# Optimization experiments

Measured on AMD Instinct MI355X. Metric: run time of the kernel, lower is better.

Reference implementation:

```python
import jax, jax.numpy as jnp
import numpy as np
import math

B, S, DM, H, F = 2, 2048, 1024, 16, 192  # F = head_dim init arg; per-head dim = F // 3
DH = F // 3
MAX_BIAS = 8.0


def _get_slopes(n):
    # faithful to ALiBiBias._get_slopes
    def pow2(n):
        start = 2.0 ** (-(2.0 ** (-(math.log2(n) - 3))))
        return [start * start ** i for i in range(n)]
    if math.log2(n).is_integer():
        return pow2(n)
    cp2 = 2 ** math.floor(math.log2(n))
    return pow2(cp2) + _get_slopes(2 * cp2)[0::2][: n - cp2]


def _rope_sin_cos(seq_len, dim):
    inv_freq = 1.0 / (10000.0 ** (jnp.arange(0, dim, 2, dtype=jnp.float32) / dim))
    freqs = jnp.outer(jnp.arange(seq_len, dtype=jnp.float32), inv_freq)  # [S, dim/2]
    # repeat(sin[:,None,:],2,axis=1).reshape(S,-1) == concat([sin,sin],-1)
    sin = jnp.concatenate([jnp.sin(freqs), jnp.sin(freqs)], axis=-1)  # [S, dim]
    cos = jnp.concatenate([jnp.cos(freqs), jnp.cos(freqs)], axis=-1)
    return sin, cos


def _rotate_half(x):
    x1, x2 = jnp.split(x, 2, axis=-1)
    return jnp.concatenate([-x2, x1], axis=-1)


def setup_inputs() -> dict:
    key = jax.random.key(0)
    kx, kq, ko = jax.random.split(key, 3)
    x = jax.random.normal(kx, (B, S, DM), dtype=jnp.float32)
    w_qkv = jax.random.normal(kq, (DM, H, F), dtype=jnp.float32) * (1.0 / math.sqrt(DM))
    b_qkv = jnp.zeros((H, F), dtype=jnp.float32)
    w_out = jax.random.normal(ko, (H, DH, DM), dtype=jnp.float32) * (1.0 / math.sqrt(H * DH))
    b_out = jnp.zeros((DM,), dtype=jnp.float32)
    return {"x": x, "w_qkv": w_qkv, "b_qkv": b_qkv, "w_out": w_out, "b_out": b_out}


def reference(x, w_qkv, b_qkv, w_out, b_out):
    b, s, dm = x.shape
    h, f = w_qkv.shape[1], w_qkv.shape[2]
    dh = f // 3
    # fused QKV projection: [B,S,H,F], then 3-way split on the feature axis
    qkv = jnp.einsum('bsd,dhf->bshf', x, w_qkv) + b_qkv
    q, k, v = jnp.split(qkv, 3, axis=-1)  # each [B,S,H,DH]
    # RoPE (rotate_half convention), broadcast over heads
    sin, cos = _rope_sin_cos(s, dh)
    sin, cos = sin[:, None, :], cos[:, None, :]  # [S,1,DH]
    q = q * cos + _rotate_half(q) * sin
    k = k * cos + _rotate_half(k) * sin
    # [B,H,S,DH]
    q = q.transpose(0, 2, 1, 3)
    k = k.transpose(0, 2, 1, 3)
    v = v.transpose(0, 2, 1, 3)
    # scores scaled by sqrt(head_dim init arg), as in the original non-flash path
    scores = jnp.einsum('bhqd,bhkd->bhqk', q, k) / jnp.sqrt(jnp.float32(f))
    # ALiBi bias
    slopes = jnp.asarray(_get_slopes(h), dtype=jnp.float32)  # [H]
    pos = jnp.arange(s, dtype=jnp.float32)
    rel = pos[None, :] - pos[:, None]  # j - i
    rel = jnp.where(rel > 0, 0.0, rel)
    alibi = rel[None, :, :] * slopes[:, None, None] * MAX_BIAS  # [H,S,S]
    scores = scores + alibi[None]  # [B,H,S,S]
    # causal mask
    causal = jnp.tril(jnp.ones((s, s), dtype=jnp.float32))
    scores = jnp.where(causal == 0, -1e9, scores)
    weights = jax.nn.softmax(scores, axis=-1)
    attn = jnp.einsum('bhqk,bhkd->bhqd', weights, v).transpose(0, 2, 1, 3)  # [B,S,H,DH]
    return jnp.einsum('bshd,hdm->bsm', attn, w_out) + b_out
```

## Files before the change

### kernel.cpp

```cpp
#include <hip/hip_runtime.h>
#include <math.h>

static constexpr int B_  = 2;
static constexpr int S_  = 2048;
static constexpr int H_  = 16;
static constexpr int DH_ = 64;
static constexpr float SCALE_ = 0.07216878364870322f;

typedef __attribute__((ext_vector_type(8))) short short8;
typedef __attribute__((ext_vector_type(4))) float floatx4;

__device__ __forceinline__ float bf2f(unsigned short u) {
    union { unsigned int i; float f; } c; c.i = ((unsigned int)u) << 16; return c.f;
}
__device__ __forceinline__ unsigned short f2bf(float f) {
    union { float f; unsigned int i; } c; c.f = f;
    unsigned int x = c.i;
    unsigned int r = (x + 0x7fffu + ((x >> 16) & 1u)) >> 16;
    if ((x & 0x7f800000u) == 0x7f800000u) r = x >> 16;
    return (unsigned short)r;
}
__device__ __forceinline__ unsigned short f2bf_pos(float f) {
    union { float f; unsigned int i; } c; c.f = f;
    return (unsigned short)((c.i + 0x7fffu + ((c.i >> 16) & 1u)) >> 16);
}
__device__ __forceinline__ void load_lds16(const unsigned short* g, unsigned short* l) {
    __builtin_amdgcn_global_load_lds(
        (const __attribute__((address_space(1))) unsigned int*)g,
        (__attribute__((address_space(3))) unsigned int*)l, 16, 0, 0);
}

__global__ __launch_bounds__(256) void cvt_x(
    const float* __restrict__ in, unsigned short* __restrict__ out)
{
    const int i = blockIdx.x * 256 + threadIdx.x;
    const float4 v = reinterpret_cast<const float4*>(in)[i];
    ushort4 r;
    r.x = f2bf(v.x); r.y = f2bf(v.y); r.z = f2bf(v.z); r.w = f2bf(v.w);
    reinterpret_cast<ushort4*>(out)[i] = r;
}

template<int NN>
__global__ __launch_bounds__(256) void transcvt(
    const float* __restrict__ in, unsigned short* __restrict__ out)
{
    __shared__ float t[32][33];
    const int n0 = blockIdx.x * 32;
    const int k0 = blockIdx.y * 32;
    const int tn = threadIdx.x & 31, tk = threadIdx.x >> 5;
    #pragma unroll
    for (int i = 0; i < 4; ++i)
        t[tk + 8 * i][tn] = in[(size_t)(k0 + tk + 8 * i) * NN + n0 + tn];
    __syncthreads();
    #pragma unroll
    for (int i = 0; i < 4; ++i)
        out[(size_t)(n0 + tk + 8 * i) * 1024 + k0 + tn] = f2bf(t[tn][tk + 8 * i]);
}

template<int NW, int MODE>
__global__ __launch_bounds__(256) void gemm_mfma(
    const unsigned short* __restrict__ A, const unsigned short* __restrict__ BT,
    const float* __restrict__ bias,
    unsigned short* __restrict__ O0, unsigned short* __restrict__ O1,
    unsigned short* __restrict__ O2, float* __restrict__ Of)
{
    __shared__ unsigned short As[128 * 32];
    __shared__ unsigned short Bs[128 * 32];

    const int tid  = threadIdx.x;
    const int wave = tid >> 6;
    const int lane = tid & 63;
    const int quad = lane >> 4;
    const int lm   = lane & 15;
    const int wm = (wave >> 1) * 64;
    const int wn = (wave & 1) * 64;
    const int n0 = blockIdx.x * 128;
    const int m0 = blockIdx.y * 128;

    floatx4 acc[4][4] = {};

    const int sr = lane >> 2;
    const int sc = lane & 3;

    for (int k0 = 0; k0 < 1024; k0 += 32) {
        #pragma unroll
        for (int rep = 0; rep < 2; ++rep) {
            const int r = wave * 32 + rep * 16;
            load_lds16(A  + (size_t)(m0 + r + sr) * 1024 + k0 + sc * 8, &As[r * 32]);
            load_lds16(BT + (size_t)(n0 + r + sr) * 1024 + k0 + sc * 8, &Bs[r * 32]);
        }
        __syncthreads();
        short8 af[4], bf[4];
        #pragma unroll
        for (int i = 0; i < 4; ++i) {
            af[i] = *reinterpret_cast<const short8*>(&As[(wm + i * 16 + lm) * 32 + quad * 8]);
            bf[i] = *reinterpret_cast<const short8*>(&Bs[(wn + i * 16 + lm) * 32 + quad * 8]);
        }
        #pragma unroll
        for (int mi = 0; mi < 4; ++mi)
            #pragma unroll
            for (int ni = 0; ni < 4; ++ni)
                acc[mi][ni] = __builtin_amdgcn_mfma_f32_16x16x32_bf16(
                    af[mi], bf[ni], acc[mi][ni], 0, 0, 0);
        __syncthreads();
    }

    if (MODE == 1) {
        #pragma unroll
        for (int ni = 0; ni < 4; ++ni) {
            const int gn = n0 + wn + ni * 16 + lm;
            const float b = bias[gn];
            #pragma unroll
            for (int mi = 0; mi < 4; ++mi) {
                const int gm = m0 + wm + mi * 16 + quad * 4;
                #pragma unroll
                for (int r = 0; r < 4; ++r)
                    Of[(size_t)(gm + r) * 1024 + gn] = acc[mi][ni][r] + b;
            }
        }
    } else {
        const int nbase = n0 + wn;
        const int h   = nbase / 192;
        const int sec = (nbase - h * 192) >> 6;
        float bia[4];
        #pragma unroll
        for (int ni = 0; ni < 4; ++ni) bia[ni] = bias[nbase + ni * 16 + lm];
        unsigned short* Out = (sec == 0) ? O0 : ((sec == 1) ? O1 : O2);
        const float qscale = (sec == 0) ? SCALE_ : 1.0f;
        const float nlf = -13.287712379549449f / 32.0f;
        const float invf0 = exp2f((float)lm * nlf);
        const float invf1 = exp2f((float)(lm + 16) * nlf);
        #pragma unroll
        for (int mi = 0; mi < 4; ++mi) {
            #pragma unroll
            for (int r = 0; r < 4; ++r) {
                const int m  = m0 + wm + mi * 16 + quad * 4 + r;
                const int bb = m >> 11;
                const int s  = m & (S_ - 1);
                const size_t obase = ((size_t)(bb * H_ + h) * S_ + s) * DH_;
                if (sec == 2) {
                    #pragma unroll
                    for (int ni = 0; ni < 4; ++ni)
                        Out[obase + ni * 16 + lm] = f2bf(acc[mi][ni][r] + bia[ni]);
                } else {
                    const float a0 = (float)s * invf0, a1 = (float)s * invf1;
                    const float sn0 = __sinf(a0), cs0 = __cosf(a0);
                    const float sn1 = __sinf(a1), cs1 = __cosf(a1);
                    #pragma unroll
                    for (int ni = 0; ni < 4; ++ni) {
                        const int d = ni * 16 + lm;
                        const float v = acc[mi][ni][r]     + bia[ni];
                        const float p = acc[mi][ni ^ 2][r] + bia[ni ^ 2];
                        const float cs = (ni & 1) ? cs1 : cs0;
                        const float sn = (ni & 1) ? sn1 : sn0;
                        float res = (d < 32) ? (v * cs - p * sn) : (v * cs + p * sn);
                        Out[obase + d] = f2bf(res * qscale);
                    }
                }
            }
        }
    }
}

static constexpr int KST = 68;
static constexpr int PST = 68;
static constexpr int VST = 70;

__global__ __launch_bounds__(256) void flash_mfma(
    const unsigned short* __restrict__ Q, const unsigned short* __restrict__ K,
    const unsigned short* __restrict__ V, unsigned short* __restrict__ Ao)
{
    __shared__ unsigned short Ks[64 * KST];
    __shared__ unsigned short VTs[64 * VST];
    __shared__ unsigned short Ps[4][16 * PST];

    const int bi = blockIdx.x;
    const int bh = bi & 31;
    const int qt = 31 - (bi >> 5);
    const int h  = bh & 15;
    const int b  = bh >> 4;
    const int tid  = threadIdx.x;
    const int wave = tid >> 6;
    const int lane = tid & 63;
    const int quad = lane >> 4;
    const int lm   = lane & 15;

    const unsigned short* Kg = K + (size_t)bh * S_ * DH_;
    const unsigned short* Vg = V + (size_t)bh * S_ * DH_;

    const unsigned short* Qrow =
        Q + ((size_t)bh * S_ + (size_t)qt * 64 + wave * 16 + lm) * DH_;
    const short8 aq0 = *reinterpret_cast<const short8*>(Qrow + quad * 8);
    const short8 aq1 = *reinterpret_cast<const short8*>(Qrow + 32 + quad * 8);

    const float slope8 = exp2f(-0.5f * (float)(h + 1)) * 8.0f;

    float l_run[4] = {};
    floatx4 acc_o[4] = {};
    unsigned short* Pw = &Ps[wave][0];

    const int srow = tid >> 2;
    const int sc8  = tid & 3;

    short8 ka, kb, va, vb2;
    {
        const unsigned short* kr = Kg + (size_t)srow * DH_ + sc8 * 8;
        ka = *reinterpret_cast<const short8*>(kr);
        kb = *reinterpret_cast<const short8*>(kr + 32);
        const unsigned short* vr = Vg + (size_t)lane * DH_ + wave * 16;
        va  = *reinterpret_cast<const short8*>(vr);
        vb2 = *reinterpret_cast<const short8*>(vr + 8);
    }

    for (int kt = 0; kt <= qt; ++kt) {
        *reinterpret_cast<short8*>(&Ks[srow * KST + sc8 * 8])      = ka;
        *reinterpret_cast<short8*>(&Ks[srow * KST + sc8 * 8 + 32]) = kb;
        #pragma unroll
        for (int j = 0; j < 8; ++j) {
            VTs[(wave * 16 + j) * VST + lane]     = (unsigned short)va[j];
            VTs[(wave * 16 + 8 + j) * VST + lane] = (unsigned short)vb2[j];
        }
        __syncthreads();

        if (kt < qt) {
            const unsigned short* kr =
                Kg + (size_t)((kt + 1) * 64 + srow) * DH_ + sc8 * 8;
            ka = *reinterpret_cast<const short8*>(kr);
            kb = *reinterpret_cast<const short8*>(kr + 32);
            const unsigned short* vr =
                Vg + (size_t)((kt + 1) * 64 + lane) * DH_ + wave * 16;
            va  = *reinterpret_cast<const short8*>(vr);
            vb2 = *reinterpret_cast<const short8*>(vr + 8);
        }

        floatx4 sacc[4] = {};
        #pragma unroll
        for (int t = 0; t < 4; ++t) {
            const short8 b0 = *reinterpret_cast<const short8*>(&Ks[(t * 16 + lm) * KST + quad * 8]);
            const short8 b1 = *reinterpret_cast<const short8*>(&Ks[(t * 16 + lm) * KST + 32 + quad * 8]);
            sacc[t] = __builtin_amdgcn_mfma_f32_16x16x32_bf16(aq0, b0, sacc[t], 0, 0, 0);
            sacc[t] = __builtin_amdgcn_mfma_f32_16x16x32_bf16(aq1, b1, sacc[t], 0, 0, 0);
        }

        const bool diag = (kt == qt);
        #pragma unroll
        for (int r = 0; r < 4; ++r) {
            const int qg = qt * 64 + wave * 16 + quad * 4 + r;
            float ps = 0.0f;
            #pragma unroll
            for (int t = 0; t < 4; ++t) {
                const int kg = kt * 64 + t * 16 + lm;
                float p = __expf(sacc[t][r] + (float)(kg - qg) * slope8 - 8.0f);
                if (diag && kg > qg) p = 0.0f;
                ps += p;
                Pw[(quad * 4 + r) * PST + t * 16 + lm] = f2bf_pos(p);
            }
            l_run[r] += ps;
        }

        const short8 ap0 = *reinterpret_cast<const short8*>(&Pw[lm * PST + quad * 8]);
        const short8 ap1 = *reinterpret_cast<const short8*>(&Pw[lm * PST + 32 + quad * 8]);
        #pragma unroll
        for (int t = 0; t < 4; ++t) {
            const short8 b0 = *reinterpret_cast<const short8*>(&VTs[(t * 16 + lm) * VST + quad * 8]);
            const short8 b1 = *reinterpret_cast<const short8*>(&VTs[(t * 16 + lm) * VST + 32 + quad * 8]);
            acc_o[t] = __builtin_amdgcn_mfma_f32_16x16x32_bf16(ap0, b0, acc_o[t], 0, 0, 0);
            acc_o[t] = __builtin_amdgcn_mfma_f32_16x16x32_bf16(ap1, b1, acc_o[t], 0, 0, 0);
        }
        __syncthreads();
    }

    #pragma unroll
    for (int r = 0; r < 4; ++r) {
        float l = l_run[r];
        l += __shfl_xor(l, 1);
        l += __shfl_xor(l, 2);
        l += __shfl_xor(l, 4);
        l += __shfl_xor(l, 8);
        const float inv_l = 1.0f / l;
        const int s = qt * 64 + wave * 16 + quad * 4 + r;
        const size_t obase = ((size_t)(b * S_ + s) * H_ + h) * DH_;
        #pragma unroll
        for (int t = 0; t < 4; ++t)
            Ao[obase + t * 16 + lm] = f2bf(acc_o[t][r] * inv_l);
    }
}

extern "C" void kernel_launch(void* const* d_in, const int* in_sizes, int n_in,
                              void* d_out, int out_size, void* d_ws, size_t ws_size,
                              hipStream_t stream)
{
    const float *x = nullptr, *w_qkv = nullptr, *b_qkv = nullptr,
                *w_out = nullptr, *b_out = nullptr;
    for (int i = 0; i < n_in; ++i) {
        switch (in_sizes[i]) {
            case 4194304: x     = (const float*)d_in[i]; break;
            case 3145728: w_qkv = (const float*)d_in[i]; break;
            case 3072:    b_qkv = (const float*)d_in[i]; break;
            case 1048576: w_out = (const float*)d_in[i]; break;
            case 1024:    b_out = (const float*)d_in[i]; break;
        }
    }
    if (!x)     x     = (const float*)d_in[0];
    if (!w_qkv) w_qkv = (const float*)d_in[1];
    if (!b_qkv) b_qkv = (const float*)d_in[2];
    if (!w_out) w_out = (const float*)d_in[3];
    if (!b_out) b_out = (const float*)d_in[4];

    float* out = (float*)d_out;
    unsigned short* ws16 = (unsigned short*)d_ws;

    unsigned short* xb     = ws16;
    unsigned short* wqkvT  = ws16 + (size_t)4194304;
    unsigned short* woutT  = ws16 + (size_t)7340032;
    unsigned short* Qb     = ws16 + (size_t)8388608;
    unsigned short* Kb     = ws16 + (size_t)12582912;
    unsigned short* Vb     = ws16 + (size_t)16777216;
    unsigned short* Aob    = ws16 + (size_t)20971520;

    cvt_x<<<4096, 256, 0, stream>>>(x, xb);
    transcvt<3072><<<dim3(96, 32), 256, 0, stream>>>(w_qkv, wqkvT);
    transcvt<1024><<<dim3(32, 32), 256, 0, stream>>>(w_out, woutT);

    gemm_mfma<3072, 0><<<dim3(24, 32), 256, 0, stream>>>(
        xb, wqkvT, b_qkv, Qb, Kb, Vb, nullptr);
    flash_mfma<<<dim3(1024), 256, 0, stream>>>(Qb, Kb, Vb, Aob);
    gemm_mfma<1024, 1><<<dim3(8, 32), 256, 0, stream>>>(
        Aob, woutT, b_out, nullptr, nullptr, nullptr, out);
}
```

Measured before the change: 214.2 us.

## Pair causal query tiles per block, store V transposed, and use exp2 with folded constants

```diff
diff --git a/kernel.cpp b/kernel.cpp
--- a/kernel.cpp
+++ b/kernel.cpp
@@ -5,7 +5,8 @@
 static constexpr int S_  = 2048;
 static constexpr int H_  = 16;
 static constexpr int DH_ = 64;
-static constexpr float SCALE_ = 0.07216878364870322f;
+static constexpr float QSCALE2_ = 0.104117589f;
+static constexpr float C8L2_    = 11.5415603f;
 
 typedef __attribute__((ext_vector_type(8))) short short8;
 typedef __attribute__((ext_vector_type(4))) float floatx4;
@@ -126,23 +127,38 @@
         #pragma unroll
         for (int ni = 0; ni < 4; ++ni) bia[ni] = bias[nbase + ni * 16 + lm];
         unsigned short* Out = (sec == 0) ? O0 : ((sec == 1) ? O1 : O2);
-        const float qscale = (sec == 0) ? SCALE_ : 1.0f;
-        const float nlf = -13.287712379549449f / 32.0f;
-        const float invf0 = exp2f((float)lm * nlf);
-        const float invf1 = exp2f((float)(lm + 16) * nlf);
-        #pragma unroll
-        for (int mi = 0; mi < 4; ++mi) {
-            #pragma unroll
-            for (int r = 0; r < 4; ++r) {
-                const int m  = m0 + wm + mi * 16 + quad * 4 + r;
+
+        if (sec == 2) {
+            #pragma unroll
+            for (int mi = 0; mi < 4; ++mi) {
+                const int m  = m0 + wm + mi * 16 + quad * 4;
                 const int bb = m >> 11;
                 const int s  = m & (S_ - 1);
-                const size_t obase = ((size_t)(bb * H_ + h) * S_ + s) * DH_;
-                if (sec == 2) {
-                    #pragma unroll
-                    for (int ni = 0; ni < 4; ++ni)
-                        Out[obase + ni * 16 + lm] = f2bf(acc[mi][ni][r] + bia[ni]);
-                } else {
+                const size_t rowb = (size_t)(bb * H_ + h) * DH_;
+                #pragma unroll
+                for (int ni = 0; ni < 4; ++ni) {
+                    const int d = ni * 16 + lm;
+                    ushort4 w;
+                    w.x = f2bf(acc[mi][ni][0] + bia[ni]);
+                    w.y = f2bf(acc[mi][ni][1] + bia[ni]);
+                    w.z = f2bf(acc[mi][ni][2] + bia[ni]);
+                    w.w = f2bf(acc[mi][ni][3] + bia[ni]);
+                    *reinterpret_cast<ushort4*>(&Out[(rowb + d) * S_ + s]) = w;
+                }
+            }
+        } else {
+            const float qscale = (sec == 0) ? QSCALE2_ : 1.0f;
+            const float nlf = -13.287712379549449f / 32.0f;
+            const float invf0 = exp2f((float)lm * nlf);
+            const float invf1 = exp2f((float)(lm + 16) * nlf);
+            #pragma unroll
+            for (int mi = 0; mi < 4; ++mi) {
+                #pragma unroll
+                for (int r = 0; r < 4; ++r) {
+                    const int m  = m0 + wm + mi * 16 + quad * 4 + r;
+                    const int bb = m >> 11;
+                    const int s  = m & (S_ - 1);
+                    const size_t obase = ((size_t)(bb * H_ + h) * S_ + s) * DH_;
                     const float a0 = (float)s * invf0, a1 = (float)s * invf1;
                     const float sn0 = __sinf(a0), cs0 = __cosf(a0);
                     const float sn1 = __sinf(a1), cs1 = __cosf(a1);
@@ -164,19 +180,18 @@
 
 static constexpr int KST = 68;
 static constexpr int PST = 68;
-static constexpr int VST = 70;
 
 __global__ __launch_bounds__(256) void flash_mfma(
     const unsigned short* __restrict__ Q, const unsigned short* __restrict__ K,
-    const unsigned short* __restrict__ V, unsigned short* __restrict__ Ao)
+    const unsigned short* __restrict__ VT, unsigned short* __restrict__ Ao)
 {
     __shared__ unsigned short Ks[64 * KST];
-    __shared__ unsigned short VTs[64 * VST];
+    __shared__ unsigned short VTs[64 * KST];
     __shared__ unsigned short Ps[4][16 * PST];
 
     const int bi = blockIdx.x;
     const int bh = bi & 31;
-    const int qt = 31 - (bi >> 5);
+    const int pr = bi >> 5;
     const int h  = bh & 15;
     const int b  = bh >> 4;
     const int tid  = threadIdx.x;
@@ -184,105 +199,118 @@
     const int lane = tid & 63;
     const int quad = lane >> 4;
     const int lm   = lane & 15;
-
-    const unsigned short* Kg = K + (size_t)bh * S_ * DH_;
-    const unsigned short* Vg = V + (size_t)bh * S_ * DH_;
-
-    const unsigned short* Qrow =
-        Q + ((size_t)bh * S_ + (size_t)qt * 64 + wave * 16 + lm) * DH_;
-    const short8 aq0 = *reinterpret_cast<const short8*>(Qrow + quad * 8);
-    const short8 aq1 = *reinterpret_cast<const short8*>(Qrow + 32 + quad * 8);
-
-    const float slope8 = exp2f(-0.5f * (float)(h + 1)) * 8.0f;
-
-    float l_run[4] = {};
-    floatx4 acc_o[4] = {};
-    unsigned short* Pw = &Ps[wave][0];
-
     const int srow = tid >> 2;
     const int sc8  = tid & 3;
 
-    short8 ka, kb, va, vb2;
-    {
-        const unsigned short* kr = Kg + (size_t)srow * DH_ + sc8 * 8;
-        ka = *reinterpret_cast<const short8*>(kr);
-        kb = *reinterpret_cast<const short8*>(kr + 32);
-        const unsigned short* vr = Vg + (size_t)lane * DH_ + wave * 16;
-        va  = *reinterpret_cast<const short8*>(vr);
-        vb2 = *reinterpret_cast<const short8*>(vr + 8);
-    }
-
-    for (int kt = 0; kt <= qt; ++kt) {
-        *reinterpret_cast<short8*>(&Ks[srow * KST + sc8 * 8])      = ka;
-        *reinterpret_cast<short8*>(&Ks[srow * KST + sc8 * 8 + 32]) = kb;
-        #pragma unroll
-        for (int j = 0; j < 8; ++j) {
-            VTs[(wave * 16 + j) * VST + lane]     = (unsigned short)va[j];
-            VTs[(wave * 16 + 8 + j) * VST + lane] = (unsigned short)vb2[j];
-        }
-        __syncthreads();
-
-        if (kt < qt) {
-            const unsigned short* kr =
-                Kg + (size_t)((kt + 1) * 64 + srow) * DH_ + sc8 * 8;
+    const unsigned short* Kg  = K  + (size_t)bh * S_ * DH_;
+    const unsigned short* VTg = VT + (size_t)bh * DH_ * S_;
+
+    const float slope2 = exp2f(-0.5f * (float)(h + 1)) * (8.0f * 1.44269504f);
+    float al[4];
+    #pragma unroll
+    for (int t = 0; t < 4; ++t) al[t] = (float)(t * 16 + lm) * slope2;
+    const float d64 = 64.0f * slope2;
+
+    unsigned short* Pw = &Ps[wave][0];
+
+    for (int ph = 0; ph < 2; ++ph) {
+        const int qt = ph ? pr : 31 - pr;
+
+        const unsigned short* Qrow =
+            Q + ((size_t)bh * S_ + (size_t)(qt * 64 + wave * 16 + lm)) * DH_;
+        const short8 aq0 = *reinterpret_cast<const short8*>(Qrow + quad * 8);
+        const short8 aq1 = *reinterpret_cast<const short8*>(Qrow + 32 + quad * 8);
+
+        const int qg = qt * 64 + wave * 16 + quad * 4;
+        float cr[4];
+        #pragma unroll
+        for (int r = 0; r < 4; ++r)
+            cr[r] = -(float)(qg + r) * slope2 - C8L2_;
+
+        float l_run[4] = {};
+        floatx4 acc_o[4] = {};
+
+        short8 ka, kb, va, vb;
+        {
+            const unsigned short* kr = Kg + (size_t)srow * DH_ + sc8 * 8;
             ka = *reinterpret_cast<const short8*>(kr);
             kb = *reinterpret_cast<const short8*>(kr + 32);
-            const unsigned short* vr =
-                Vg + (size_t)((kt + 1) * 64 + lane) * DH_ + wave * 16;
-            va  = *reinterpret_cast<const short8*>(vr);
-            vb2 = *reinterpret_cast<const short8*>(vr + 8);
-        }
-
-        floatx4 sacc[4] = {};
-        #pragma unroll
-        for (int t = 0; t < 4; ++t) {
-            const short8 b0 = *reinterpret_cast<const short8*>(&Ks[(t * 16 + lm) * KST + quad * 8]);
-            const short8 b1 = *reinterpret_cast<const short8*>(&Ks[(t * 16 + lm) * KST + 32 + quad * 8]);
-            sacc[t] = __builtin_amdgcn_mfma_f32_16x16x32_bf16(aq0, b0, sacc[t], 0, 0, 0);
-            sacc[t] = __builtin_amdgcn_mfma_f32_16x16x32_bf16(aq1, b1, sacc[t], 0, 0, 0);
-        }
-
-        const bool diag = (kt == qt);
+            const unsigned short* vr = VTg + (size_t)srow * S_ + sc8 * 8;
+            va = *reinterpret_cast<const short8*>(vr);
+            vb = *reinterpret_cast<const short8*>(vr + 32);
+        }
+
+        for (int kt = 0; kt <= qt; ++kt) {
+            *reinterpret_cast<short8*>(&Ks[srow * KST + sc8 * 8])       = ka;
+            *reinterpret_cast<short8*>(&Ks[srow * KST + sc8 * 8 + 32])  = kb;
+            *reinterpret_cast<short8*>(&VTs[srow * KST + sc8 * 8])      = va;
+            *reinterpret_cast<short8*>(&VTs[srow * KST + sc8 * 8 + 32]) = vb;
+            __syncthreads();
+
+            if (kt < qt) {
+                const unsigned short* kr =
+                    Kg + (size_t)((kt + 1) * 64 + srow) * DH_ + sc8 * 8;
+                ka = *reinterpret_cast<const short8*>(kr);
+                kb = *reinterpret_cast<const short8*>(kr + 32);
+                const unsigned short* vr =
+                    VTg + (size_t)srow * S_ + (kt + 1) * 64 + sc8 * 8;
+                va = *reinterpret_cast<const short8*>(vr);
+                vb = *reinterpret_cast<const short8*>(vr + 32);
+            }
+
+            floatx4 sacc[4] = {};
+            #pragma unroll
+            for (int t = 0; t < 4; ++t) {
+                const short8 b0 = *reinterpret_cast<const short8*>(&Ks[(t * 16 + lm) * KST + quad * 8]);
+                const short8 b1 = *reinterpret_cast<const short8*>(&Ks[(t * 16 + lm) * KST + 32 + quad * 8]);
+                sacc[t] = __builtin_amdgcn_mfma_f32_16x16x32_bf16(aq0, b0, sacc[t], 0, 0, 0);
+                sacc[t] = __builtin_amdgcn_mfma_f32_16x16x32_bf16(aq1, b1, sacc[t], 0, 0, 0);
+            }
+
+            const bool diag = (kt == qt);
+            #pragma unroll
+            for (int r = 0; r < 4; ++r) {
+                float ps = 0.0f;
+                #pragma unroll
+                for (int t = 0; t < 4; ++t) {
+                    const float x = (sacc[t][r] + al[t]) + cr[r];
+                    float p;
+                    asm("v_exp_f32 %0, %1" : "=v"(p) : "v"(x));
+                    if (diag && (kt * 64 + t * 16 + lm) > (qg + r)) p = 0.0f;
+                    ps += p;
+                    Pw[(quad * 4 + r) * PST + t * 16 + lm] = f2bf_pos(p);
+                }
+                l_run[r] += ps;
+            }
+            #pragma unroll
+            for (int r = 0; r < 4; ++r) cr[r] += d64;
+
+            const short8 ap0 = *reinterpret_cast<const short8*>(&Pw[lm * PST + quad * 8]);
+            const short8 ap1 = *reinterpret_cast<const short8*>(&Pw[lm * PST + 32 + quad * 8]);
+            #pragma unroll
+            for (int t = 0; t < 4; ++t) {
+                const short8 b0 = *reinterpret_cast<const short8*>(&VTs[(t * 16 + lm) * KST + quad * 8]);
+                const short8 b1 = *reinterpret_cast<const short8*>(&VTs[(t * 16 + lm) * KST + 32 + quad * 8]);
+                acc_o[t] = __builtin_amdgcn_mfma_f32_16x16x32_bf16(ap0, b0, acc_o[t], 0, 0, 0);
+                acc_o[t] = __builtin_amdgcn_mfma_f32_16x16x32_bf16(ap1, b1, acc_o[t], 0, 0, 0);
+            }
+            __syncthreads();
+        }
+
         #pragma unroll
         for (int r = 0; r < 4; ++r) {
-            const int qg = qt * 64 + wave * 16 + quad * 4 + r;
-            float ps = 0.0f;
-            #pragma unroll
-            for (int t = 0; t < 4; ++t) {
-                const int kg = kt * 64 + t * 16 + lm;
-                float p = __expf(sacc[t][r] + (float)(kg - qg) * slope8 - 8.0f);
-                if (diag && kg > qg) p = 0.0f;
-                ps += p;
-                Pw[(quad * 4 + r) * PST + t * 16 + lm] = f2bf_pos(p);
-            }
-            l_run[r] += ps;
-        }
-
-        const short8 ap0 = *reinterpret_cast<const short8*>(&Pw[lm * PST + quad * 8]);
-        const short8 ap1 = *reinterpret_cast<const short8*>(&Pw[lm * PST + 32 + quad * 8]);
-        #pragma unroll
-        for (int t = 0; t < 4; ++t) {
-            const short8 b0 = *reinterpret_cast<const short8*>(&VTs[(t * 16 + lm) * VST + quad * 8]);
-            const short8 b1 = *reinterpret_cast<const short8*>(&VTs[(t * 16 + lm) * VST + 32 + quad * 8]);
-            acc_o[t] = __builtin_amdgcn_mfma_f32_16x16x32_bf16(ap0, b0, acc_o[t], 0, 0, 0);
-            acc_o[t] = __builtin_amdgcn_mfma_f32_16x16x32_bf16(ap1, b1, acc_o[t], 0, 0, 0);
-        }
-        __syncthreads();
-    }
-
-    #pragma unroll
-    for (int r = 0; r < 4; ++r) {
-        float l = l_run[r];
-        l += __shfl_xor(l, 1);
-        l += __shfl_xor(l, 2);
-        l += __shfl_xor(l, 4);
-        l += __shfl_xor(l, 8);
-        const float inv_l = 1.0f / l;
-        const int s = qt * 64 + wave * 16 + quad * 4 + r;
-        const size_t obase = ((size_t)(b * S_ + s) * H_ + h) * DH_;
-        #pragma unroll
-        for (int t = 0; t < 4; ++t)
-            Ao[obase + t * 16 + lm] = f2bf(acc_o[t][r] * inv_l);
+            float l = l_run[r];
+            l += __shfl_xor(l, 1);
+            l += __shfl_xor(l, 2);
+            l += __shfl_xor(l, 4);
+            l += __shfl_xor(l, 8);
+            const float inv_l = 1.0f / l;
+            const int s = qg + r;
+            const size_t obase = ((size_t)(b * S_ + s) * H_ + h) * DH_;
+            #pragma unroll
+            for (int t = 0; t < 4; ++t)
+                Ao[obase + t * 16 + lm] = f2bf(acc_o[t][r] * inv_l);
+        }
     }
 }
 
@@ -324,7 +352,7 @@
 
     gemm_mfma<3072, 0><<<dim3(24, 32), 256, 0, stream>>>(
         xb, wqkvT, b_qkv, Qb, Kb, Vb, nullptr);
-    flash_mfma<<<dim3(1024), 256, 0, stream>>>(Qb, Kb, Vb, Aob);
+    flash_mfma<<<dim3(512), 256, 0, stream>>>(Qb, Kb, Vb, Aob);
     gemm_mfma<1024, 1><<<dim3(8, 32), 256, 0, stream>>>(
         Aob, woutT, b_out, nullptr, nullptr, nullptr, out);
 }
```

After: 204.9 us. 4.3% less time.
